# Kernel optimization log

Hardware: AMD Instinct MI355X
Metric: run time of the kernel (lower is better)

The kernel has to match this reference:

```python
import jax, jax.numpy as jnp
import numpy as np

FRAME = 1024; HOP = 256; HID = 128; ENC = 256; FREQ = FRAME // 2 + 1  # 513
B = 16; T = 262144


def _gru(x, h0, Wih, Whh, bih, bhh):
    # x: [B, T, I], h0: [B, H]; torch GRU gate order: r, z, n
    H = h0.shape[-1]
    xg = jnp.einsum('bti,gi->btg', x, Wih) + bih  # [B, T, 3H]
    def step(h, g):
        gh = h @ Whh.T + bhh
        r = jax.nn.sigmoid(g[:, :H] + gh[:, :H])
        z = jax.nn.sigmoid(g[:, H:2 * H] + gh[:, H:2 * H])
        n = jnp.tanh(g[:, 2 * H:] + r * gh[:, 2 * H:])
        hn = (1.0 - z) * n + z * h
        return hn, hn
    h_last, ys = jax.lax.scan(step, h0, jnp.swapaxes(xg, 0, 1))
    return jnp.swapaxes(ys, 0, 1), h_last


def _sep(x, states, Wih1, Whh1, bih1, bhh1, Wih2, Whh2, bih2, bhh2, Wd, bd):
    x1, s1 = _gru(x, states[0], Wih1, Whh1, bih1, bhh1)
    x2, s2 = _gru(x1, states[1], Wih2, Whh2, bih2, bhh2)
    mask = jax.nn.sigmoid(jnp.einsum('bth,oh->bto', x2, Wd) + bd)
    return mask, jnp.stack([s1, s2])


def _dtln(x, in_state1, in_state2,
          s1_Wih1, s1_Whh1, s1_bih1, s1_bhh1, s1_Wih2, s1_Whh2, s1_bih2, s1_bhh2, s1_Wd, s1_bd,
          enc_W, gamma, beta,
          s2_Wih1, s2_Whh1, s2_bih1, s2_bhh1, s2_Wih2, s2_Whh2, s2_bih2, s2_bhh2, s2_Wd, s2_bd,
          dec_W):
    eps = jnp.finfo(jnp.float32).eps
    Bn, Tn = x.shape
    nF = (Tn - FRAME) // HOP + 1
    # periodic hann window (torch.hann_window default)
    win = (0.5 * (1.0 - jnp.cos(2.0 * jnp.pi * jnp.arange(FRAME) / FRAME))).astype(jnp.float32)
    idx = jnp.arange(nF)[:, None] * HOP + jnp.arange(FRAME)[None, :]  # [F, FRAME]
    frames = x[:, idx] * win                     # [B, F, FRAME]
    spec = jnp.fft.rfft(frames, axis=-1)         # [B, F, FREQ] complex64
    re, im = spec.real, spec.imag
    mag = jnp.sqrt(jnp.clip(re * re + im * im, eps))
    phase = jnp.arctan2(im + eps, re + eps)
    # separation block 1 on magnitude
    mask1, out_state1 = _sep(mag, in_state1, s1_Wih1, s1_Whh1, s1_bih1, s1_bhh1,
                             s1_Wih2, s1_Whh2, s1_bih2, s1_bhh2, s1_Wd, s1_bd)
    est_mag = mask1 * mag
    s1_stft = est_mag * jnp.exp(1j * phase)
    y1 = jnp.fft.irfft(s1_stft, n=FRAME, axis=-1)  # [B, F, FRAME]
    # 1x1 conv encoder == per-frame matmul
    encoded = jnp.einsum('bfk,ek->bfe', y1, enc_W)  # [B, F, ENC]
    # instant layer norm over channels
    mean = jnp.mean(encoded, axis=-1, keepdims=True)
    var = jnp.mean(jnp.square(encoded - mean), axis=-1, keepdims=True)
    enc_norm = (encoded - mean) / jnp.sqrt(var + 1e-7) * gamma + beta
    # separation block 2 in learned feature domain
    mask2, out_state2 = _sep(enc_norm, in_state2, s2_Wih1, s2_Whh1, s2_bih1, s2_bhh1,
                             s2_Wih2, s2_Whh2, s2_bih2, s2_bhh2, s2_Wd, s2_bd)
    est2 = mask2 * encoded
    dec = jnp.einsum('bfe,ke->bfk', est2, dec_W)   # [B, F, FRAME]
    # overlap-add (torch fold with output size (T,1))
    out = jnp.zeros((Bn, Tn), dtype=x.dtype).at[:, idx].add(dec)
    return out, out_state1, out_state2


def setup_inputs() -> dict:
    key = jax.random.key(0)
    ks = jax.random.split(key, 24)
    def nrm(k, shape, s=0.08):
        return (jax.random.normal(k, shape) * s).astype(jnp.float32)
    H3 = 3 * HID
    return {
        'x': (jax.random.normal(ks[0], (B, T)) * 0.1).astype(jnp.float32),
        'in_state1': jnp.zeros((2, B, HID), jnp.float32),
        'in_state2': jnp.zeros((2, B, HID), jnp.float32),
        's1_Wih1': nrm(ks[1], (H3, FREQ)), 's1_Whh1': nrm(ks[2], (H3, HID)),
        's1_bih1': nrm(ks[3], (H3,)), 's1_bhh1': nrm(ks[4], (H3,)),
        's1_Wih2': nrm(ks[5], (H3, HID)), 's1_Whh2': nrm(ks[6], (H3, HID)),
        's1_bih2': nrm(ks[7], (H3,)), 's1_bhh2': nrm(ks[8], (H3,)),
        's1_Wd': nrm(ks[9], (FREQ, HID)), 's1_bd': nrm(ks[10], (FREQ,)),
        'enc_W': nrm(ks[11], (ENC, FRAME)),
        'gamma': jnp.ones((1, 1, ENC), jnp.float32),
        'beta': jnp.zeros((1, 1, ENC), jnp.float32),
        's2_Wih1': nrm(ks[12], (H3, ENC)), 's2_Whh1': nrm(ks[13], (H3, HID)),
        's2_bih1': nrm(ks[14], (H3,)), 's2_bhh1': nrm(ks[15], (H3,)),
        's2_Wih2': nrm(ks[16], (H3, HID)), 's2_Whh2': nrm(ks[17], (H3, HID)),
        's2_bih2': nrm(ks[18], (H3,)), 's2_bhh2': nrm(ks[19], (H3,)),
        's2_Wd': nrm(ks[20], (ENC, HID)), 's2_bd': nrm(ks[21], (ENC,)),
        'dec_W': nrm(ks[22], (FRAME, ENC)),
    }


def reference(x, in_state1, in_state2,
              s1_Wih1, s1_Whh1, s1_bih1, s1_bhh1, s1_Wih2, s1_Whh2, s1_bih2, s1_bhh2, s1_Wd, s1_bd,
              enc_W, gamma, beta,
              s2_Wih1, s2_Whh1, s2_bih1, s2_bhh1, s2_Wih2, s2_Whh2, s2_bih2, s2_bhh2, s2_Wd, s2_bd,
              dec_W):
    return _dtln(x, in_state1, in_state2,
                 s1_Wih1, s1_Whh1, s1_bih1, s1_bhh1, s1_Wih2, s1_Whh2, s1_bih2, s1_bhh2, s1_Wd, s1_bd,
                 enc_W, gamma, beta,
                 s2_Wih1, s2_Whh1, s2_bih1, s2_bhh1, s2_Wih2, s2_Whh2, s2_bih2, s2_bhh2, s2_Wd, s2_bd,
                 dec_W)
```

## Files before the change

### kernel.cpp

```cpp
#include <hip/hip_runtime.h>
#include <math.h>

#define F_FRAMES 1021
#define BATCH 16
#define T_LEN 262144
#define FREQn 513
#define HID 128
#define ENCn 256
#define BF (BATCH * F_FRAMES)

__device__ __forceinline__ float sigmoidf_(float x) {
  return 1.f / (1.f + __expf(-x));
}
__device__ __forceinline__ float tanhf_(float x) {
  return 1.f - 2.f / (__expf(2.f * x) + 1.f);
}

__global__ __launch_bounds__(256) void stft_kernel(
    const float* __restrict__ x, float* __restrict__ mag,
    float* __restrict__ cosp, float* __restrict__ sinp) {
  __shared__ float zr[512], zi[512];
  int bf = blockIdx.x;
  int b = bf / F_FRAMES;
  int f = bf - b * F_FRAMES;
  const float* xb = x + (size_t)b * T_LEN + (size_t)f * 256;
  int tid = threadIdx.x;
  const float wstep = 6.28318530717958647692f / 1024.f;
#pragma unroll
  for (int u = 0; u < 2; ++u) {
    int j = tid + u * 256;
    int n = __brev((unsigned)j) >> 23;
    float x0 = xb[2 * n] * (0.5f - 0.5f * __cosf((float)(2 * n) * wstep));
    float x1 = xb[2 * n + 1] * (0.5f - 0.5f * __cosf((float)(2 * n + 1) * wstep));
    zr[j] = x0;
    zi[j] = x1;
  }
  __syncthreads();
#pragma unroll
  for (int s = 1; s <= 9; ++s) {
    int half = 1 << (s - 1);
    int t = tid & (half - 1);
    int g = tid >> (s - 1);
    int pos = (g << s) + t;
    float ang = (float)t * (3.14159265358979323846f / (float)half);
    float sn, cs;
    __sincosf(ang, &sn, &cs);
    float wr = cs, wi = -sn;
    float ar = zr[pos], ai = zi[pos];
    float br = zr[pos + half], bi = zi[pos + half];
    float tr = wr * br - wi * bi;
    float ti = wr * bi + wi * br;
    zr[pos] = ar + tr;
    zi[pos] = ai + ti;
    zr[pos + half] = ar - tr;
    zi[pos + half] = ai - ti;
    __syncthreads();
  }
  const float eps = 1.1920928955078125e-07f;
  for (int k = tid; k < 513; k += 256) {
    int ka = k & 511;
    int kb = (512 - k) & 511;
    float zar = zr[ka], zai = zi[ka];
    float zbr = zr[kb], zbi = zi[kb];
    float Zer = 0.5f * (zar + zbr);
    float Zei = 0.5f * (zai - zbi);
    float Zor = 0.5f * (zai + zbi);
    float Zoi = -0.5f * (zar - zbr);
    float ang = (float)k * (3.14159265358979323846f / 512.f);
    float sn, cs;
    __sincosf(ang, &sn, &cs);
    float Wr = cs, Wi = -sn;
    float re = Zer + Wr * Zor - Wi * Zoi;
    float im = Zei + Wr * Zoi + Wi * Zor;
    size_t idx = (size_t)bf * FREQn + k;
    float p2 = re * re + im * im;
    mag[idx] = sqrtf(fmaxf(p2, eps));
    float rr = re + eps, ii = im + eps;
    float inv = rsqrtf(rr * rr + ii * ii);
    cosp[idx] = rr * inv;
    sinp[idx] = ii * inv;
  }
}

__global__ __launch_bounds__(256) void istft_kernel(
    const float* __restrict__ er, const float* __restrict__ ei,
    float* __restrict__ y) {
  __shared__ float xr[513], xi[513];
  __shared__ float zr[512], zi[512];
  int bf = blockIdx.x;
  int tid = threadIdx.x;
  for (int k = tid; k < 513; k += 256) {
    size_t idx = (size_t)bf * FREQn + k;
    xr[k] = er[idx];
    float v = ei[idx];
    xi[k] = (k == 0 || k == 512) ? 0.f : v;
  }
  __syncthreads();
#pragma unroll
  for (int u = 0; u < 2; ++u) {
    int k = tid + u * 256;
    int kk = 512 - k;
    float Xkr = xr[k], Xki = xi[k];
    float Xbr = xr[kk], Xbi = xi[kk];
    float Zer = 0.5f * (Xkr + Xbr);
    float Zei = 0.5f * (Xki - Xbi);
    float Vr = 0.5f * (Xkr - Xbr);
    float Vi = 0.5f * (Xki + Xbi);
    float ang = (float)k * (3.14159265358979323846f / 512.f);
    float sn, cs;
    __sincosf(ang, &sn, &cs);
    float Zor = cs * Vr - sn * Vi;
    float Zoi = cs * Vi + sn * Vr;
    float Rr = Zer - Zoi;
    float Ri = Zei + Zor;
    int d = __brev((unsigned)k) >> 23;
    zr[d] = Rr;
    zi[d] = Ri;
  }
  __syncthreads();
#pragma unroll
  for (int s = 1; s <= 9; ++s) {
    int half = 1 << (s - 1);
    int t = tid & (half - 1);
    int g = tid >> (s - 1);
    int pos = (g << s) + t;
    float ang = (float)t * (3.14159265358979323846f / (float)half);
    float sn, cs;
    __sincosf(ang, &sn, &cs);
    float wr = cs, wi = sn;
    float ar = zr[pos], ai = zi[pos];
    float br = zr[pos + half], bi = zi[pos + half];
    float tr = wr * br - wi * bi;
    float ti = wr * bi + wi * br;
    zr[pos] = ar + tr;
    zi[pos] = ai + ti;
    zr[pos + half] = ar - tr;
    zi[pos + half] = ai - ti;
    __syncthreads();
  }
  const float sc = 1.f / 512.f;
  float2* y2 = (float2*)(y + (size_t)bf * 1024);
#pragma unroll
  for (int u = 0; u < 2; ++u) {
    int n = tid + u * 256;
    y2[n] = make_float2(zr[n] * sc, zi[n] * sc);
  }
}

template <int MODE>
__global__ __launch_bounds__(256) void gemm_nt(
    const float* __restrict__ A, const float* __restrict__ W,
    const float* __restrict__ bias, float* __restrict__ C, int M, int N, int K,
    const float* __restrict__ aux1, float* __restrict__ aux2,
    float* __restrict__ aux3) {
  __shared__ float As[16][68];
  __shared__ float Ws[16][68];
  int tid = threadIdx.x;
  int tx = tid & 15, ty = tid >> 4;
  int m0 = blockIdx.y * 64, n0 = blockIdx.x * 64;
  float acc[4][4] = {};
  int klc = tid & 15;
  int rl = tid >> 4;
  for (int k0 = 0; k0 < K; k0 += 16) {
#pragma unroll
    for (int r = 0; r < 4; ++r) {
      int row = rl + r * 16;
      int m = m0 + row;
      int k = k0 + klc;
      As[klc][row] = (m < M && k < K) ? A[(size_t)m * K + k] : 0.f;
      int n = n0 + row;
      Ws[klc][row] = (n < N && k < K) ? W[(size_t)n * K + k] : 0.f;
    }
    __syncthreads();
#pragma unroll
    for (int kk = 0; kk < 16; ++kk) {
      float4 a4 = *reinterpret_cast<const float4*>(&As[kk][ty * 4]);
      float4 w4 = *reinterpret_cast<const float4*>(&Ws[kk][tx * 4]);
      float av[4] = {a4.x, a4.y, a4.z, a4.w};
      float wv[4] = {w4.x, w4.y, w4.z, w4.w};
#pragma unroll
      for (int i = 0; i < 4; ++i)
#pragma unroll
        for (int j = 0; j < 4; ++j)
          acc[i][j] = fmaf(av[i], wv[j], acc[i][j]);
    }
    __syncthreads();
  }
#pragma unroll
  for (int i = 0; i < 4; ++i) {
    int m = m0 + ty * 4 + i;
    if (m >= M) continue;
#pragma unroll
    for (int j = 0; j < 4; ++j) {
      int n = n0 + tx * 4 + j;
      if (n >= N) continue;
      float v = acc[i][j];
      if (bias) v += bias[n];
      size_t idx = (size_t)m * N + n;
      if (MODE == 0) {
        C[idx] = v;
      } else if (MODE == 1) {
        float s = sigmoidf_(v);
        float em = s * aux1[idx];
        aux2[idx] = em * aux2[idx];
        aux3[idx] = em * aux3[idx];
      } else {
        float s = sigmoidf_(v);
        C[idx] = s * aux1[idx];
      }
    }
  }
}

__global__ __launch_bounds__(384) void gru_scan(
    const float* __restrict__ xg,
    const float* __restrict__ Whh,
    const float* __restrict__ bhh,
    const float* __restrict__ h0,
    float* __restrict__ hout,
    float* __restrict__ hlast,
    int F) {
  __shared__ float h_s[128];
  __shared__ float a_s[384];
  __shared__ float xn_s[128];
  int b = blockIdx.x;
  int g = threadIdx.x;
  float w[128];
#pragma unroll
  for (int k = 0; k < 128; ++k) w[k] = Whh[g * 128 + k];
  float bh = bhh[g];
  if (g < 128) h_s[g] = h0[b * 128 + g];
  __syncthreads();
  const float* xgb = xg + (size_t)b * F * 384;
  float* hob = hout + (size_t)b * F * 128;
  for (int t = 0; t < F; ++t) {
    float xv = xgb[(size_t)t * 384 + g];
    float ac0 = 0.f, ac1 = 0.f, ac2 = 0.f, ac3 = 0.f;
#pragma unroll
    for (int k = 0; k < 128; k += 4) {
      ac0 = fmaf(w[k], h_s[k], ac0);
      ac1 = fmaf(w[k + 1], h_s[k + 1], ac1);
      ac2 = fmaf(w[k + 2], h_s[k + 2], ac2);
      ac3 = fmaf(w[k + 3], h_s[k + 3], ac3);
    }
    float acc = bh + ((ac0 + ac1) + (ac2 + ac3));
    if (g < 256) {
      a_s[g] = xv + acc;
    } else {
      a_s[g] = acc;
      xn_s[g - 256] = xv;
    }
    __syncthreads();
    if (g < 128) {
      float r = sigmoidf_(a_s[g]);
      float z = sigmoidf_(a_s[128 + g]);
      float nv = tanhf_(xn_s[g] + r * a_s[256 + g]);
      float hn = (1.f - z) * nv + z * h_s[g];
      h_s[g] = hn;
      hob[(size_t)t * 128 + g] = hn;
    }
    __syncthreads();
  }
  if (g < 128) hlast[b * 128 + g] = h_s[g];
}

__global__ __launch_bounds__(256) void ln_kernel(
    const float* __restrict__ enc, const float* __restrict__ gamma,
    const float* __restrict__ beta, float* __restrict__ out) {
  int row = blockIdx.x * 4 + (threadIdx.x >> 6);
  int lane = threadIdx.x & 63;
  const float* p = enc + (size_t)row * ENCn;
  float4 v = *reinterpret_cast<const float4*>(p + lane * 4);
  float s = v.x + v.y + v.z + v.w;
  float ss = v.x * v.x + v.y * v.y + v.z * v.z + v.w * v.w;
#pragma unroll
  for (int o = 32; o > 0; o >>= 1) {
    s += __shfl_down(s, o);
    ss += __shfl_down(ss, o);
  }
  s = __shfl(s, 0);
  ss = __shfl(ss, 0);
  float mean = s * (1.f / 256.f);
  float var = ss * (1.f / 256.f) - mean * mean;
  float rstd = rsqrtf(var + 1e-7f);
  float4 g4 = *reinterpret_cast<const float4*>(gamma + lane * 4);
  float4 b4 = *reinterpret_cast<const float4*>(beta + lane * 4);
  float4 o4;
  o4.x = (v.x - mean) * rstd * g4.x + b4.x;
  o4.y = (v.y - mean) * rstd * g4.y + b4.y;
  o4.z = (v.z - mean) * rstd * g4.z + b4.z;
  o4.w = (v.w - mean) * rstd * g4.w + b4.w;
  *reinterpret_cast<float4*>(out + (size_t)row * ENCn + lane * 4) = o4;
}

__global__ __launch_bounds__(256) void ola_kernel(const float* __restrict__ dec,
                                                  float* __restrict__ out) {
  int idx = blockIdx.x * 256 + threadIdx.x;
  int b = idx >> 18;
  int n = idx & (T_LEN - 1);
  int f0 = (n < 768) ? 0 : ((n - 768) >> 8);
  int f1 = min(n >> 8, F_FRAMES - 1);
  float s = 0.f;
  for (int f = f0; f <= f1; ++f)
    s += dec[((size_t)b * F_FRAMES + f) * 1024 + (n - (f << 8))];
  out[idx] = s;
}

extern "C" void kernel_launch(void* const* d_in, const int* in_sizes, int n_in,
                              void* d_out, int out_size, void* d_ws,
                              size_t ws_size, hipStream_t stream) {
  const float* x = (const float*)d_in[0];
  const float* in_st1 = (const float*)d_in[1];
  const float* in_st2 = (const float*)d_in[2];
  const float* s1_Wih1 = (const float*)d_in[3];
  const float* s1_Whh1 = (const float*)d_in[4];
  const float* s1_bih1 = (const float*)d_in[5];
  const float* s1_bhh1 = (const float*)d_in[6];
  const float* s1_Wih2 = (const float*)d_in[7];
  const float* s1_Whh2 = (const float*)d_in[8];
  const float* s1_bih2 = (const float*)d_in[9];
  const float* s1_bhh2 = (const float*)d_in[10];
  const float* s1_Wd = (const float*)d_in[11];
  const float* s1_bd = (const float*)d_in[12];
  const float* enc_W = (const float*)d_in[13];
  const float* gamma = (const float*)d_in[14];
  const float* beta = (const float*)d_in[15];
  const float* s2_Wih1 = (const float*)d_in[16];
  const float* s2_Whh1 = (const float*)d_in[17];
  const float* s2_bih1 = (const float*)d_in[18];
  const float* s2_bhh1 = (const float*)d_in[19];
  const float* s2_Wih2 = (const float*)d_in[20];
  const float* s2_Whh2 = (const float*)d_in[21];
  const float* s2_bih2 = (const float*)d_in[22];
  const float* s2_bhh2 = (const float*)d_in[23];
  const float* s2_Wd = (const float*)d_in[24];
  const float* s2_bd = (const float*)d_in[25];
  const float* dec_W = (const float*)d_in[26];

  float* out = (float*)d_out;
  float* st_out = out + (size_t)BATCH * T_LEN;

  float* ws = (float*)d_ws;
  float* mag = ws;
  float* cosp = mag + (size_t)BF * FREQn;
  float* sinp = cosp + (size_t)BF * FREQn;
  float* xgA = sinp + (size_t)BF * FREQn;
  float* xgB = xgA + (size_t)BF * 384;
  float* h1 = xgB + (size_t)BF * 384;
  float* h2 = h1 + (size_t)BF * HID;
  float* ybuf = h2 + (size_t)BF * HID;
  float* enc = ybuf + (size_t)BF * 1024;
  float* encn = enc + (size_t)BF * ENCn;

  auto gg = [](int M, int N) { return dim3((N + 63) / 64, (M + 63) / 64); };

  stft_kernel<<<BF, 256, 0, stream>>>(x, mag, cosp, sinp);
  gemm_nt<0><<<gg(BF, 384), 256, 0, stream>>>(mag, s1_Wih1, s1_bih1, xgA, BF,
                                              384, FREQn, nullptr, nullptr,
                                              nullptr);
  gru_scan<<<BATCH, 384, 0, stream>>>(xgA, s1_Whh1, s1_bhh1, in_st1, h1,
                                      st_out, F_FRAMES);
  gemm_nt<0><<<gg(BF, 384), 256, 0, stream>>>(h1, s1_Wih2, s1_bih2, xgB, BF,
                                              384, HID, nullptr, nullptr,
                                              nullptr);
  gru_scan<<<BATCH, 384, 0, stream>>>(xgB, s1_Whh2, s1_bhh2, in_st1 + 2048, h2,
                                      st_out + 2048, F_FRAMES);
  gemm_nt<1><<<gg(BF, FREQn), 256, 0, stream>>>(h2, s1_Wd, s1_bd, nullptr, BF,
                                                FREQn, HID, mag, cosp, sinp);
  istft_kernel<<<BF, 256, 0, stream>>>(cosp, sinp, ybuf);
  gemm_nt<0><<<gg(BF, ENCn), 256, 0, stream>>>(ybuf, enc_W, nullptr, enc, BF,
                                               ENCn, 1024, nullptr, nullptr,
                                               nullptr);
  ln_kernel<<<BF / 4, 256, 0, stream>>>(enc, gamma, beta, encn);
  gemm_nt<0><<<gg(BF, 384), 256, 0, stream>>>(encn, s2_Wih1, s2_bih1, xgA, BF,
                                              384, ENCn, nullptr, nullptr,
                                              nullptr);
  gru_scan<<<BATCH, 384, 0, stream>>>(xgA, s2_Whh1, s2_bhh1, in_st2, h1,
                                      st_out + 4096, F_FRAMES);
  gemm_nt<0><<<gg(BF, 384), 256, 0, stream>>>(h1, s2_Wih2, s2_bih2, xgB, BF,
                                              384, HID, nullptr, nullptr,
                                              nullptr);
  gru_scan<<<BATCH, 384, 0, stream>>>(xgB, s2_Whh2, s2_bhh2, in_st2 + 2048, h2,
                                      st_out + 6144, F_FRAMES);
  gemm_nt<2><<<gg(BF, ENCn), 256, 0, stream>>>(h2, s2_Wd, s2_bd, encn, BF,
                                               ENCn, HID, enc, nullptr,
                                               nullptr);
  gemm_nt<0><<<gg(BF, 1024), 256, 0, stream>>>(encn, dec_W, nullptr, ybuf, BF,
                                               1024, ENCn, nullptr, nullptr,
                                               nullptr);
  ola_kernel<<<(BATCH * T_LEN) / 256, 256, 0, stream>>>(ybuf, out);
}
```

Before: 4.294 ms.

## Split GRU recurrent dot product across thread pairs with vectorized LDS reads

The recurrent GRU scan now uses 768 threads per batch, with two threads per gate row. Each thread holds half of the Whh row (64 floats) in registers and reads h as float4 from LDS, and the two partial sums are combined with a lane shuffle. The input-gate value for the next step is prefetched a step ahead. The aim is to shorten the serial per-timestep latency and relieve register pressure in this latency-bound scan, at the cost of an extra shuffle and more waves taking part in each barrier.

Measured after the change: 5.518 ms. 28.5% more time.

```diff
diff --git a/kernel.cpp b/kernel.cpp
--- a/kernel.cpp
+++ b/kernel.cpp
@@ -8,6 +8,8 @@
 #define HID 128
 #define ENCn 256
 #define BF (BATCH * F_FRAMES)
+
+typedef float v4f __attribute__((ext_vector_type(4)));
 
 __device__ __forceinline__ float sigmoidf_(float x) {
   return 1.f / (1.f + __expf(-x));
@@ -212,7 +214,7 @@
   }
 }
 
-__global__ __launch_bounds__(384) void gru_scan(
+__global__ __launch_bounds__(768, 3) void gru_scan(
     const float* __restrict__ xg,
     const float* __restrict__ Whh,
     const float* __restrict__ bhh,
@@ -220,48 +222,62 @@
     float* __restrict__ hout,
     float* __restrict__ hlast,
     int F) {
-  __shared__ float h_s[128];
+  __shared__ __align__(16) float h_s[128];
   __shared__ float a_s[384];
   __shared__ float xn_s[128];
   int b = blockIdx.x;
-  int g = threadIdx.x;
-  float w[128];
-#pragma unroll
-  for (int k = 0; k < 128; ++k) w[k] = Whh[g * 128 + k];
-  float bh = bhh[g];
-  if (g < 128) h_s[g] = h0[b * 128 + g];
+  int tid = threadIdx.x;
+  int row = tid >> 1;
+  int half = tid & 1;
+  const float* wrow = Whh + (size_t)row * 128 + half * 64;
+  v4f w[16];
+#pragma unroll
+  for (int k = 0; k < 16; ++k)
+    w[k] = *reinterpret_cast<const v4f*>(wrow + 4 * k);
+#pragma unroll
+  for (int k = 0; k < 16; ++k) asm volatile("" : "+v"(w[k]));
+  float bh = (half == 0) ? bhh[row] : 0.f;
+  if (tid < 128) h_s[tid] = h0[b * 128 + tid];
+  const float* xgb = xg + (size_t)b * F * 384 + row;
+  float* hob = hout + (size_t)b * F * 128;
+  float xv_cur = (half == 0) ? xgb[0] : 0.f;
   __syncthreads();
-  const float* xgb = xg + (size_t)b * F * 384;
-  float* hob = hout + (size_t)b * F * 128;
   for (int t = 0; t < F; ++t) {
-    float xv = xgb[(size_t)t * 384 + g];
-    float ac0 = 0.f, ac1 = 0.f, ac2 = 0.f, ac3 = 0.f;
-#pragma unroll
-    for (int k = 0; k < 128; k += 4) {
-      ac0 = fmaf(w[k], h_s[k], ac0);
-      ac1 = fmaf(w[k + 1], h_s[k + 1], ac1);
-      ac2 = fmaf(w[k + 2], h_s[k + 2], ac2);
-      ac3 = fmaf(w[k + 3], h_s[k + 3], ac3);
-    }
-    float acc = bh + ((ac0 + ac1) + (ac2 + ac3));
-    if (g < 256) {
-      a_s[g] = xv + acc;
-    } else {
-      a_s[g] = acc;
-      xn_s[g - 256] = xv;
-    }
-    __syncthreads();
-    if (g < 128) {
-      float r = sigmoidf_(a_s[g]);
-      float z = sigmoidf_(a_s[128 + g]);
-      float nv = tanhf_(xn_s[g] + r * a_s[256 + g]);
-      float hn = (1.f - z) * nv + z * h_s[g];
-      h_s[g] = hn;
-      hob[(size_t)t * 128 + g] = hn;
-    }
-    __syncthreads();
-  }
-  if (g < 128) hlast[b * 128 + g] = h_s[g];
+    float xv_nxt = (half == 0 && t + 1 < F) ? xgb[(size_t)(t + 1) * 384] : 0.f;
+    const v4f* h4 = reinterpret_cast<const v4f*>(h_s + half * 64);
+    v4f a0 = {0.f, 0.f, 0.f, 0.f}, a1 = a0, a2 = a0, a3 = a0;
+#pragma unroll
+    for (int k = 0; k < 16; k += 4) {
+      a0 = __builtin_elementwise_fma(w[k + 0], h4[k + 0], a0);
+      a1 = __builtin_elementwise_fma(w[k + 1], h4[k + 1], a1);
+      a2 = __builtin_elementwise_fma(w[k + 2], h4[k + 2], a2);
+      a3 = __builtin_elementwise_fma(w[k + 3], h4[k + 3], a3);
+    }
+    v4f sv = (a0 + a1) + (a2 + a3);
+    float s = (sv.x + sv.y) + (sv.z + sv.w);
+    s += __shfl_xor(s, 1);
+    if (half == 0) {
+      float acc = bh + s;
+      if (row < 256) {
+        a_s[row] = xv_cur + acc;
+      } else {
+        a_s[row] = acc;
+        xn_s[row - 256] = xv_cur;
+      }
+    }
+    __syncthreads();
+    if (tid < 128) {
+      float r = sigmoidf_(a_s[tid]);
+      float z = sigmoidf_(a_s[128 + tid]);
+      float nv = tanhf_(xn_s[tid] + r * a_s[256 + tid]);
+      float hn = (1.f - z) * nv + z * h_s[tid];
+      h_s[tid] = hn;
+      hob[(size_t)t * 128 + tid] = hn;
+    }
+    xv_cur = xv_nxt;
+    __syncthreads();
+  }
+  if (tid < 128) hlast[b * 128 + tid] = h_s[tid];
 }
 
 __global__ __launch_bounds__(256) void ln_kernel(
@@ -358,12 +374,12 @@
   gemm_nt<0><<<gg(BF, 384), 256, 0, stream>>>(mag, s1_Wih1, s1_bih1, xgA, BF,
                                               384, FREQn, nullptr, nullptr,
                                               nullptr);
-  gru_scan<<<BATCH, 384, 0, stream>>>(xgA, s1_Whh1, s1_bhh1, in_st1, h1,
+  gru_scan<<<BATCH, 768, 0, stream>>>(xgA, s1_Whh1, s1_bhh1, in_st1, h1,
                                       st_out, F_FRAMES);
   gemm_nt<0><<<gg(BF, 384), 256, 0, stream>>>(h1, s1_Wih2, s1_bih2, xgB, BF,
                                               384, HID, nullptr, nullptr,
                                               nullptr);
-  gru_scan<<<BATCH, 384, 0, stream>>>(xgB, s1_Whh2, s1_bhh2, in_st1 + 2048, h2,
+  gru_scan<<<BATCH, 768, 0, stream>>>(xgB, s1_Whh2, s1_bhh2, in_st1 + 2048, h2,
                                       st_out + 2048, F_FRAMES);
   gemm_nt<1><<<gg(BF, FREQn), 256, 0, stream>>>(h2, s1_Wd, s1_bd, nullptr, BF,
                                                 FREQn, HID, mag, cosp, sinp);
@@ -375,12 +391,12 @@
   gemm_nt<0><<<gg(BF, 384), 256, 0, stream>>>(encn, s2_Wih1, s2_bih1, xgA, BF,
                                               384, ENCn, nullptr, nullptr,
                                               nullptr);
-  gru_scan<<<BATCH, 384, 0, stream>>>(xgA, s2_Whh1, s2_bhh1, in_st2, h1,
+  gru_scan<<<BATCH, 768, 0, stream>>>(xgA, s2_Whh1, s2_bhh1, in_st2, h1,
                                       st_out + 4096, F_FRAMES);
   gemm_nt<0><<<gg(BF, 384), 256, 0, stream>>>(h1, s2_Wih2, s2_bih2, xgB, BF,
                                               384, HID, nullptr, nullptr,
                                               nullptr);
-  gru_scan<<<BATCH, 384, 0, stream>>>(xgB, s2_Whh2, s2_bhh2, in_st2 + 2048, h2,
+  gru_scan<<<BATCH, 768, 0, stream>>>(xgB, s2_Whh2, s2_bhh2, in_st2 + 2048, h2,
                                       st_out + 6144, F_FRAMES);
   gemm_nt<2><<<gg(BF, ENCn), 256, 0, stream>>>(h2, s2_Wd, s2_bd, encn, BF,
                                                ENCn, HID, enc, nullptr,
```

## Run GRU recurrence with split-fp16 MFMA across all batches in one block

Applied to the files above, without the earlier changes.

Replaces the per-batch scalar GRU scan, which used one block per batch element with 384 threads each doing a 128-long dot product, with a single 512-thread block. Each step computes the hidden-to-hidden matmul for all 16 batch rows using 16x16x32 f16 MFMA. The weights are pre-split into hi/lo fp16 parts by a new prep kernel so accuracy stays close to fp32. The hidden state is double-buffered in shared memory to need one barrier per step, and the input-gate values are prefetched two steps ahead. The trade-off is running on a single CU with twice the MFMA work for the hi/lo split, in exchange for a much shorter per-step latency chain.

Measured after the change: 7.848 ms. +82.8%, slower.

```diff
diff --git a/kernel.cpp b/kernel.cpp
--- a/kernel.cpp
+++ b/kernel.cpp
@@ -8,6 +8,10 @@
 #define HID 128
 #define ENCn 256
 #define BF (BATCH * F_FRAMES)
+
+typedef float v4f __attribute__((ext_vector_type(4)));
+typedef _Float16 f16x8 __attribute__((ext_vector_type(8)));
+typedef _Float16 f16x4 __attribute__((ext_vector_type(4)));
 
 __device__ __forceinline__ float sigmoidf_(float x) {
   return 1.f / (1.f + __expf(-x));
@@ -212,56 +216,125 @@
   }
 }
 
-__global__ __launch_bounds__(384) void gru_scan(
+__global__ __launch_bounds__(256) void prep_wfrag(
+    const float* __restrict__ W0, const float* __restrict__ W1,
+    const float* __restrict__ W2, const float* __restrict__ W3,
+    _Float16* __restrict__ out) {
+  int idx = blockIdx.x * 256 + threadIdx.x;
+  if (idx >= 4 * 98304) return;
+  int j = idx & 7;
+  int lane = (idx >> 3) & 63;
+  int prec = (idx >> 9) & 1;
+  int k = (idx >> 10) & 3;
+  int rest = idx >> 12;
+  int mat = rest / 24;
+  int wg = rest % 24;
+  int w = wg / 3, g = wg % 3;
+  const float* W = mat == 0 ? W0 : mat == 1 ? W1 : mat == 2 ? W2 : W3;
+  int row = g * 128 + w * 16 + (lane & 15);
+  int col = k * 32 + (lane >> 4) * 8 + j;
+  float v = W[row * 128 + col];
+  _Float16 hi = (_Float16)v;
+  out[idx] = prec ? (_Float16)(v - (float)hi) : hi;
+}
+
+__global__ __launch_bounds__(512, 2)
+__attribute__((amdgpu_waves_per_eu(2, 2))) void gru_scan_mfma(
     const float* __restrict__ xg,
-    const float* __restrict__ Whh,
+    const _Float16* __restrict__ wf,
     const float* __restrict__ bhh,
     const float* __restrict__ h0,
     float* __restrict__ hout,
     float* __restrict__ hlast,
     int F) {
-  __shared__ float h_s[128];
-  __shared__ float a_s[384];
-  __shared__ float xn_s[128];
-  int b = blockIdx.x;
-  int g = threadIdx.x;
-  float w[128];
-#pragma unroll
-  for (int k = 0; k < 128; ++k) w[k] = Whh[g * 128 + k];
-  float bh = bhh[g];
-  if (g < 128) h_s[g] = h0[b * 128 + g];
+  __shared__ __align__(16) _Float16 HT[2][16][136];
+  int tid = threadIdx.x;
+  int wv = tid >> 6, l = tid & 63;
+  int n = l & 15;
+  int rq = l >> 4;
+  int rbase = wv * 16 + rq * 4;
+
+  f16x8 whi[3][4], wlo[3][4];
+  const f16x8* fb = (const f16x8*)wf;
+#pragma unroll
+  for (int g = 0; g < 3; ++g)
+#pragma unroll
+    for (int k = 0; k < 4; ++k) {
+      whi[g][k] = fb[(((wv * 3 + g) * 4 + k) * 2 + 0) * 64 + l];
+      wlo[g][k] = fb[(((wv * 3 + g) * 4 + k) * 2 + 1) * 64 + l];
+    }
+  float bhr[4], bhz[4], bhn[4];
+#pragma unroll
+  for (int r = 0; r < 4; ++r) {
+    bhr[r] = bhh[rbase + r];
+    bhz[r] = bhh[128 + rbase + r];
+    bhn[r] = bhh[256 + rbase + r];
+  }
+  float hp[4];
+#pragma unroll
+  for (int r = 0; r < 4; ++r) {
+    hp[r] = h0[n * 128 + rbase + r];
+    HT[0][n][rbase + r] = (_Float16)hp[r];
+  }
+  const float* xp = xg + ((size_t)n * F) * 384 + rbase;
+  float* hq = hout + ((size_t)n * F) * 128 + rbase;
+  v4f xra = *(const v4f*)(xp);
+  v4f xza = *(const v4f*)(xp + 128);
+  v4f xna = *(const v4f*)(xp + 256);
+  const float* p1 = xp + (size_t)(F > 1 ? 1 : 0) * 384;
+  v4f xrb = *(const v4f*)(p1);
+  v4f xzb = *(const v4f*)(p1 + 128);
+  v4f xnb = *(const v4f*)(p1 + 256);
   __syncthreads();
-  const float* xgb = xg + (size_t)b * F * 384;
-  float* hob = hout + (size_t)b * F * 128;
+
+  int cur = 0;
   for (int t = 0; t < F; ++t) {
-    float xv = xgb[(size_t)t * 384 + g];
-    float ac0 = 0.f, ac1 = 0.f, ac2 = 0.f, ac3 = 0.f;
-#pragma unroll
-    for (int k = 0; k < 128; k += 4) {
-      ac0 = fmaf(w[k], h_s[k], ac0);
-      ac1 = fmaf(w[k + 1], h_s[k + 1], ac1);
-      ac2 = fmaf(w[k + 2], h_s[k + 2], ac2);
-      ac3 = fmaf(w[k + 3], h_s[k + 3], ac3);
-    }
-    float acc = bh + ((ac0 + ac1) + (ac2 + ac3));
-    if (g < 256) {
-      a_s[g] = xv + acc;
-    } else {
-      a_s[g] = acc;
-      xn_s[g - 256] = xv;
-    }
+    const _Float16* hrow = &HT[cur][n][0];
+    f16x8 b0 = *(const f16x8*)(hrow + rq * 8);
+    f16x8 b1 = *(const f16x8*)(hrow + 32 + rq * 8);
+    f16x8 b2 = *(const f16x8*)(hrow + 64 + rq * 8);
+    f16x8 b3 = *(const f16x8*)(hrow + 96 + rq * 8);
+    v4f xr = xra, xz = xza, xn = xna;
+    xra = xrb; xza = xzb; xna = xnb;
+    {
+      int tp = (t + 2 < F) ? t + 2 : F - 1;
+      const float* p2 = xp + (size_t)tp * 384;
+      xrb = *(const v4f*)(p2);
+      xzb = *(const v4f*)(p2 + 128);
+      xnb = *(const v4f*)(p2 + 256);
+    }
+    v4f ar = {0.f, 0.f, 0.f, 0.f}, az = ar, an = ar;
+#pragma unroll
+    for (int k = 0; k < 4; ++k) {
+      f16x8 bk = (k == 0) ? b0 : (k == 1) ? b1 : (k == 2) ? b2 : b3;
+      ar = __builtin_amdgcn_mfma_f32_16x16x32_f16(whi[0][k], bk, ar, 0, 0, 0);
+      az = __builtin_amdgcn_mfma_f32_16x16x32_f16(whi[1][k], bk, az, 0, 0, 0);
+      an = __builtin_amdgcn_mfma_f32_16x16x32_f16(whi[2][k], bk, an, 0, 0, 0);
+      ar = __builtin_amdgcn_mfma_f32_16x16x32_f16(wlo[0][k], bk, ar, 0, 0, 0);
+      az = __builtin_amdgcn_mfma_f32_16x16x32_f16(wlo[1][k], bk, az, 0, 0, 0);
+      an = __builtin_amdgcn_mfma_f32_16x16x32_f16(wlo[2][k], bk, an, 0, 0, 0);
+    }
+    int nxt = cur ^ 1;
+    f16x4 hv;
+    v4f ho;
+#pragma unroll
+    for (int r = 0; r < 4; ++r) {
+      float rr = sigmoidf_(ar[r] + bhr[r] + xr[r]);
+      float zz = sigmoidf_(az[r] + bhz[r] + xz[r]);
+      float gn = an[r] + bhn[r];
+      float nv = tanhf_(xn[r] + rr * gn);
+      float hn = (1.f - zz) * nv + zz * hp[r];
+      hp[r] = hn;
+      hv[r] = (_Float16)hn;
+      ho[r] = hn;
+    }
+    *(f16x4*)&HT[nxt][n][rbase] = hv;
+    *(v4f*)(hq + (size_t)t * 128) = ho;
     __syncthreads();
-    if (g < 128) {
-      float r = sigmoidf_(a_s[g]);
-      float z = sigmoidf_(a_s[128 + g]);
-      float nv = tanhf_(xn_s[g] + r * a_s[256 + g]);
-      float hn = (1.f - z) * nv + z * h_s[g];
-      h_s[g] = hn;
-      hob[(size_t)t * 128 + g] = hn;
-    }
-    __syncthreads();
-  }
-  if (g < 128) hlast[b * 128 + g] = h_s[g];
+    cur = nxt;
+  }
+#pragma unroll
+  for (int r = 0; r < 4; ++r) hlast[n * 128 + rbase + r] = hp[r];
 }
 
 __global__ __launch_bounds__(256) void ln_kernel(
@@ -344,27 +417,30 @@
   float* mag = ws;
   float* cosp = mag + (size_t)BF * FREQn;
   float* sinp = cosp + (size_t)BF * FREQn;
-  float* xgA = sinp + (size_t)BF * FREQn;
-  float* xgB = xgA + (size_t)BF * 384;
-  float* h1 = xgB + (size_t)BF * 384;
+  float* xg = sinp + (size_t)BF * FREQn;
+  float* h1 = xg + (size_t)BF * 384;
   float* h2 = h1 + (size_t)BF * HID;
   float* ybuf = h2 + (size_t)BF * HID;
   float* enc = ybuf + (size_t)BF * 1024;
   float* encn = enc + (size_t)BF * ENCn;
+  _Float16* wfrag = (_Float16*)(encn + (size_t)BF * ENCn);
 
   auto gg = [](int M, int N) { return dim3((N + 63) / 64, (M + 63) / 64); };
 
+  prep_wfrag<<<1536, 256, 0, stream>>>(s1_Whh1, s1_Whh2, s2_Whh1, s2_Whh2,
+                                       wfrag);
   stft_kernel<<<BF, 256, 0, stream>>>(x, mag, cosp, sinp);
-  gemm_nt<0><<<gg(BF, 384), 256, 0, stream>>>(mag, s1_Wih1, s1_bih1, xgA, BF,
+  gemm_nt<0><<<gg(BF, 384), 256, 0, stream>>>(mag, s1_Wih1, s1_bih1, xg, BF,
                                               384, FREQn, nullptr, nullptr,
                                               nullptr);
-  gru_scan<<<BATCH, 384, 0, stream>>>(xgA, s1_Whh1, s1_bhh1, in_st1, h1,
-                                      st_out, F_FRAMES);
-  gemm_nt<0><<<gg(BF, 384), 256, 0, stream>>>(h1, s1_Wih2, s1_bih2, xgB, BF,
+  gru_scan_mfma<<<1, 512, 0, stream>>>(xg, wfrag + 0 * 98304, s1_bhh1, in_st1,
+                                       h1, st_out, F_FRAMES);
+  gemm_nt<0><<<gg(BF, 384), 256, 0, stream>>>(h1, s1_Wih2, s1_bih2, xg, BF,
                                               384, HID, nullptr, nullptr,
                                               nullptr);
-  gru_scan<<<BATCH, 384, 0, stream>>>(xgB, s1_Whh2, s1_bhh2, in_st1 + 2048, h2,
-                                      st_out + 2048, F_FRAMES);
+  gru_scan_mfma<<<1, 512, 0, stream>>>(xg, wfrag + 1 * 98304, s1_bhh2,
+                                       in_st1 + 2048, h2, st_out + 2048,
+                                       F_FRAMES);
   gemm_nt<1><<<gg(BF, FREQn), 256, 0, stream>>>(h2, s1_Wd, s1_bd, nullptr, BF,
                                                 FREQn, HID, mag, cosp, sinp);
   istft_kernel<<<BF, 256, 0, stream>>>(cosp, sinp, ybuf);
@@ -372,16 +448,17 @@
                                                ENCn, 1024, nullptr, nullptr,
                                                nullptr);
   ln_kernel<<<BF / 4, 256, 0, stream>>>(enc, gamma, beta, encn);
-  gemm_nt<0><<<gg(BF, 384), 256, 0, stream>>>(encn, s2_Wih1, s2_bih1, xgA, BF,
+  gemm_nt<0><<<gg(BF, 384), 256, 0, stream>>>(encn, s2_Wih1, s2_bih1, xg, BF,
                                               384, ENCn, nullptr, nullptr,
                                               nullptr);
-  gru_scan<<<BATCH, 384, 0, stream>>>(xgA, s2_Whh1, s2_bhh1, in_st2, h1,
-                                      st_out + 4096, F_FRAMES);
-  gemm_nt<0><<<gg(BF, 384), 256, 0, stream>>>(h1, s2_Wih2, s2_bih2, xgB, BF,
+  gru_scan_mfma<<<1, 512, 0, stream>>>(xg, wfrag + 2 * 98304, s2_bhh1, in_st2,
+                                       h1, st_out + 4096, F_FRAMES);
+  gemm_nt<0><<<gg(BF, 384), 256, 0, stream>>>(h1, s2_Wih2, s2_bih2, xg, BF,
                                               384, HID, nullptr, nullptr,
                                               nullptr);
-  gru_scan<<<BATCH, 384, 0, stream>>>(xgB, s2_Whh2, s2_bhh2, in_st2 + 2048, h2,
-                                      st_out + 6144, F_FRAMES);
+  gru_scan_mfma<<<1, 512, 0, stream>>>(xg, wfrag + 3 * 98304, s2_bhh2,
+                                       in_st2 + 2048, h2, st_out + 6144,
+                                       F_FRAMES);
   gemm_nt<2><<<gg(BF, ENCn), 256, 0, stream>>>(h2, s2_Wd, s2_bd, encn, BF,
                                                ENCn, HID, enc, nullptr,
                                                nullptr);
```
